# Kernel optimization log

Measured on AMD Instinct MI355X. Metric: run time of the kernel, lower is better.

## Reference

```python
import jax, jax.numpy as jnp
import numpy as np

NUM_INPUTS = 8
NUM_MFS = 3
NUM_RULES = NUM_MFS ** NUM_INPUTS  # 6561
BATCH = 8192


def setup_inputs() -> dict:
    key = jax.random.key(0)
    k1, k2, k3 = jax.random.split(key, 3)
    x = jax.random.normal(k1, (BATCH, NUM_INPUTS), dtype=jnp.float32)
    # one GaussianMF per input: centers ~ randn(num_mfs)
    centers = jax.random.normal(k2, (NUM_INPUTS, NUM_MFS), dtype=jnp.float32)
    # sigmas fixed buffer [0.3, 0.5, 0.7] shared across all inputs
    sigmas = jnp.array([0.3, 0.5, 0.7], dtype=jnp.float32)
    consequents = jax.random.normal(k3, (NUM_RULES, NUM_INPUTS + 1), dtype=jnp.float32)
    return {"x": x, "centers": centers, "sigmas": sigmas, "consequents": consequents}


def reference(x, centers, sigmas, consequents):
    B, nI = x.shape
    M = centers.shape[1]
    # Gaussian memberships: [B, nI, M]
    mu = jnp.exp(-0.5 * ((x[:, :, None] - centers[None, :, :]) / sigmas[None, None, :]) ** 2)
    # Rule strengths via successive outer products (lexicographic order matches
    # itertools.product(range(M), repeat=nI): first input varies slowest).
    s = mu[:, 0, :]  # [B, M]
    for j in range(1, nI):
        s = (s[:, :, None] * mu[:, j, None, :]).reshape(B, -1)  # [B, M^(j+1)]
    # s: [B, NUM_RULES]
    ones = jnp.ones((B, 1), dtype=x.dtype)
    xb = jnp.concatenate([x, ones], axis=1)  # [B, nI+1]
    rule_outputs = jnp.einsum('bi,ri->br', xb, consequents)  # [B, R]
    out = jnp.sum(s * rule_outputs, axis=1) / (jnp.sum(s, axis=1) + 1e-6)
    return out[:, None]
```

## Files before the change

### kernel.cpp

```cpp
#include <hip/hip_runtime.h>
#include <math.h>

#define BATCH   8192
#define NI      8
#define NM      3
#define NR      6561
#define NROWS   81
#define NL      81

__device__ __forceinline__ float sel3(const float* a, int i) {
    return (i == 0) ? a[0] : ((i == 1) ? a[1] : a[2]);
}

__global__ __launch_bounds__(256, 8) void sugeno_partial(
    const float* __restrict__ x,
    const float* __restrict__ centers,
    const float* __restrict__ sigmas,
    const float* __restrict__ cons,
    float* __restrict__ partial,
    int nchunk)
{
    const int b     = blockIdx.x * 256 + threadIdx.x;
    const int chunk = blockIdx.y;

    const float4* xv = reinterpret_cast<const float4*>(x + (size_t)b * NI);
    float4 xa = xv[0], xb4 = xv[1];
    float xr[NI];
    xr[0]=xa.x; xr[1]=xa.y; xr[2]=xa.z; xr[3]=xa.w;
    xr[4]=xb4.x; xr[5]=xb4.y; xr[6]=xb4.z; xr[7]=xb4.w;

    float inv[NM];
    #pragma unroll
    for (int m = 0; m < NM; ++m) {
        float s = sigmas[m];
        inv[m] = -0.5f / (s * s);
    }

    float mu[NI][NM];
    #pragma unroll
    for (int j = 0; j < NI; ++j) {
        #pragma unroll
        for (int m = 0; m < NM; ++m) {
            float d = xr[j] - centers[j * NM + m];
            mu[j][m] = __expf(d * d * inv[m]);
        }
    }

    const int rH0 = (chunk * NROWS) / nchunk;
    const int rH1 = ((chunk + 1) * NROWS) / nchunk;

    float V[9];
    #pragma unroll
    for (int i = 0; i < 9; ++i) V[i] = 0.0f;

    for (int rH = rH0; rH < rH1; ++rH) {
        int d0 = rH / 27, rem = rH - d0 * 27;
        int d1 = rem / 9;  rem -= d1 * 9;
        int d2 = rem / 3;
        int d3 = rem - d2 * 3;
        const float ph = sel3(mu[0], d0) * sel3(mu[1], d1)
                       * sel3(mu[2], d2) * sel3(mu[3], d3);
        const float* __restrict__ crow = cons + (size_t)rH * NL * 9;

        #pragma unroll
        for (int m4 = 0; m4 < 3; ++m4) {
            const float p4 = ph * mu[4][m4];
            #pragma unroll
            for (int m5 = 0; m5 < 3; ++m5) {
                const float p5 = p4 * mu[5][m5];
                #pragma unroll
                for (int m6 = 0; m6 < 3; ++m6) {
                    const float p6 = p5 * mu[6][m6];
                    #pragma unroll
                    for (int m7 = 0; m7 < 3; ++m7) {
                        const float s = p6 * mu[7][m7];
                        const float* cr = crow + (size_t)((((m4*3+m5)*3+m6)*3)+m7) * 9;
                        #pragma unroll
                        for (int i = 0; i < 9; ++i) V[i] += s * cr[i];
                    }
                }
            }
        }
    }

    const float numer = V[0]*xr[0] + V[1]*xr[1] + V[2]*xr[2] + V[3]*xr[3]
                      + V[4]*xr[4] + V[5]*xr[5] + V[6]*xr[6] + V[7]*xr[7]
                      + V[8];
    partial[(size_t)chunk * BATCH + b] = numer;
}

__global__ __launch_bounds__(256) void sugeno_reduce(
    const float* __restrict__ x,
    const float* __restrict__ centers,
    const float* __restrict__ sigmas,
    const float* __restrict__ partial,
    float* __restrict__ out,
    int nchunk)
{
    const int b = blockIdx.x * blockDim.x + threadIdx.x;
    if (b >= BATCH) return;

    const float4* xv = reinterpret_cast<const float4*>(x + (size_t)b * NI);
    float4 xa = xv[0], xb4 = xv[1];
    float xr[NI];
    xr[0]=xa.x; xr[1]=xa.y; xr[2]=xa.z; xr[3]=xa.w;
    xr[4]=xb4.x; xr[5]=xb4.y; xr[6]=xb4.z; xr[7]=xb4.w;

    float inv[NM];
    #pragma unroll
    for (int m = 0; m < NM; ++m) {
        float s = sigmas[m];
        inv[m] = -0.5f / (s * s);
    }

    float denom = 1.0f;
    #pragma unroll
    for (int j = 0; j < NI; ++j) {
        float srow = 0.0f;
        #pragma unroll
        for (int m = 0; m < NM; ++m) {
            float d = xr[j] - centers[j * NM + m];
            srow += __expf(d * d * inv[m]);
        }
        denom *= srow;
    }

    float numer = 0.0f;
    #pragma unroll 4
    for (int k = 0; k < nchunk; ++k)
        numer += partial[(size_t)k * BATCH + b];

    out[b] = numer / (denom + 1e-6f);
}

extern "C" void kernel_launch(void* const* d_in, const int* in_sizes, int n_in,
                              void* d_out, int out_size, void* d_ws, size_t ws_size,
                              hipStream_t stream)
{
    const float* x       = (const float*)d_in[0];
    const float* centers = (const float*)d_in[1];
    const float* sigmas  = (const float*)d_in[2];
    const float* cons    = (const float*)d_in[3];
    float* out           = (float*)d_out;
    float* partial       = (float*)d_ws;

    int nchunk = (int)(ws_size / ((size_t)BATCH * sizeof(float)));
    if (nchunk > NROWS) nchunk = NROWS;
    if (nchunk < 1)     nchunk = 1;

    dim3 grid1(BATCH / 256, nchunk, 1);
    sugeno_partial<<<grid1, dim3(256, 1, 1), 0, stream>>>(x, centers, sigmas, cons,
                                                          partial, nchunk);

    dim3 grid2(BATCH / 256, 1, 1);
    sugeno_reduce<<<grid2, dim3(256, 1, 1), 0, stream>>>(x, centers, sigmas,
                                                         partial, out, nchunk);
}
```

Before: 27.87 us.

## Fix one rule-row per block and split partial reduction across waves

The partial kernel now always launches 81 row-chunks (one high-order rule row per block), so each thread computes only the memberships it needs for that row instead of all 24 exponentials and the selection logic. Exponentials use exp2f with a pre-scaled constant. The reduce kernel spreads the 81-way sum over four waves per block and combines them through shared memory, giving more parallelism in the reduction. The change assumes the workspace can always hold 81 partial rows; the old code capped the chunk count by workspace size, and it writes more partial data than before.

```diff
diff --git a/kernel.cpp b/kernel.cpp
--- a/kernel.cpp
+++ b/kernel.cpp
@@ -4,24 +4,19 @@
 #define BATCH   8192
 #define NI      8
 #define NM      3
-#define NR      6561
 #define NROWS   81
 #define NL      81
+#define IL2C    (-0.72134752f)
 
-__device__ __forceinline__ float sel3(const float* a, int i) {
-    return (i == 0) ? a[0] : ((i == 1) ? a[1] : a[2]);
-}
-
-__global__ __launch_bounds__(256, 8) void sugeno_partial(
+__global__ __launch_bounds__(256) void sugeno_partial(
     const float* __restrict__ x,
     const float* __restrict__ centers,
     const float* __restrict__ sigmas,
     const float* __restrict__ cons,
-    float* __restrict__ partial,
-    int nchunk)
+    float* __restrict__ partial)
 {
-    const int b     = blockIdx.x * 256 + threadIdx.x;
-    const int chunk = blockIdx.y;
+    const int b  = blockIdx.x * 256 + threadIdx.x;
+    const int rH = blockIdx.y;
 
     const float4* xv = reinterpret_cast<const float4*>(x + (size_t)b * NI);
     float4 xa = xv[0], xb4 = xv[1];
@@ -29,55 +24,59 @@
     xr[0]=xa.x; xr[1]=xa.y; xr[2]=xa.z; xr[3]=xa.w;
     xr[4]=xb4.x; xr[5]=xb4.y; xr[6]=xb4.z; xr[7]=xb4.w;
 
-    float inv[NM];
+    float il2[NM];
     #pragma unroll
     for (int m = 0; m < NM; ++m) {
         float s = sigmas[m];
-        inv[m] = -0.5f / (s * s);
+        il2[m] = IL2C / (s * s);
     }
 
-    float mu[NI][NM];
+    const int d0 = rH / 27;
+    const int d1 = (rH / 9) % 3;
+    const int d2 = (rH / 3) % 3;
+    const int d3 = rH % 3;
+
+    float dd0 = xr[0] - centers[0 * NM + d0];
+    float dd1 = xr[1] - centers[1 * NM + d1];
+    float dd2 = xr[2] - centers[2 * NM + d2];
+    float dd3 = xr[3] - centers[3 * NM + d3];
+    float ph = exp2f(dd0 * dd0 * il2[d0]) * exp2f(dd1 * dd1 * il2[d1])
+             * exp2f(dd2 * dd2 * il2[d2]) * exp2f(dd3 * dd3 * il2[d3]);
+
+    float mu4[NM], mu5[NM], mu6[NM], mu7[NM];
     #pragma unroll
-    for (int j = 0; j < NI; ++j) {
-        #pragma unroll
-        for (int m = 0; m < NM; ++m) {
-            float d = xr[j] - centers[j * NM + m];
-            mu[j][m] = __expf(d * d * inv[m]);
-        }
+    for (int m = 0; m < NM; ++m) {
+        float e4 = xr[4] - centers[4 * NM + m];
+        float e5 = xr[5] - centers[5 * NM + m];
+        float e6 = xr[6] - centers[6 * NM + m];
+        float e7 = xr[7] - centers[7 * NM + m];
+        mu4[m] = exp2f(e4 * e4 * il2[m]);
+        mu5[m] = exp2f(e5 * e5 * il2[m]);
+        mu6[m] = exp2f(e6 * e6 * il2[m]);
+        mu7[m] = exp2f(e7 * e7 * il2[m]);
     }
 
-    const int rH0 = (chunk * NROWS) / nchunk;
-    const int rH1 = ((chunk + 1) * NROWS) / nchunk;
+    const float* __restrict__ crow = cons + (size_t)rH * NL * 9;
 
     float V[9];
     #pragma unroll
     for (int i = 0; i < 9; ++i) V[i] = 0.0f;
 
-    for (int rH = rH0; rH < rH1; ++rH) {
-        int d0 = rH / 27, rem = rH - d0 * 27;
-        int d1 = rem / 9;  rem -= d1 * 9;
-        int d2 = rem / 3;
-        int d3 = rem - d2 * 3;
-        const float ph = sel3(mu[0], d0) * sel3(mu[1], d1)
-                       * sel3(mu[2], d2) * sel3(mu[3], d3);
-        const float* __restrict__ crow = cons + (size_t)rH * NL * 9;
-
+    #pragma unroll
+    for (int m4 = 0; m4 < 3; ++m4) {
+        const float p4 = ph * mu4[m4];
         #pragma unroll
-        for (int m4 = 0; m4 < 3; ++m4) {
-            const float p4 = ph * mu[4][m4];
+        for (int m5 = 0; m5 < 3; ++m5) {
+            const float p5 = p4 * mu5[m5];
             #pragma unroll
-            for (int m5 = 0; m5 < 3; ++m5) {
-                const float p5 = p4 * mu[5][m5];
+            for (int m6 = 0; m6 < 3; ++m6) {
+                const float p6 = p5 * mu6[m6];
                 #pragma unroll
-                for (int m6 = 0; m6 < 3; ++m6) {
-                    const float p6 = p5 * mu[6][m6];
+                for (int m7 = 0; m7 < 3; ++m7) {
+                    const float s = p6 * mu7[m7];
+                    const float* cr = crow + (size_t)((((m4*3+m5)*3+m6)*3)+m7) * 9;
                     #pragma unroll
-                    for (int m7 = 0; m7 < 3; ++m7) {
-                        const float s = p6 * mu[7][m7];
-                        const float* cr = crow + (size_t)((((m4*3+m5)*3+m6)*3)+m7) * 9;
-                        #pragma unroll
-                        for (int i = 0; i < 9; ++i) V[i] += s * cr[i];
-                    }
+                    for (int i = 0; i < 9; ++i) V[i] += s * cr[i];
                 }
             }
         }
@@ -86,7 +85,7 @@
     const float numer = V[0]*xr[0] + V[1]*xr[1] + V[2]*xr[2] + V[3]*xr[3]
                       + V[4]*xr[4] + V[5]*xr[5] + V[6]*xr[6] + V[7]*xr[7]
                       + V[8];
-    partial[(size_t)chunk * BATCH + b] = numer;
+    partial[(size_t)rH * BATCH + b] = numer;
 }
 
 __global__ __launch_bounds__(256) void sugeno_reduce(
@@ -94,43 +93,49 @@
     const float* __restrict__ centers,
     const float* __restrict__ sigmas,
     const float* __restrict__ partial,
-    float* __restrict__ out,
-    int nchunk)
+    float* __restrict__ out)
 {
-    const int b = blockIdx.x * blockDim.x + threadIdx.x;
-    if (b >= BATCH) return;
+    __shared__ float red[4][64];
+    const int lane = threadIdx.x & 63;
+    const int w    = threadIdx.x >> 6;
+    const int b    = blockIdx.x * 64 + lane;
 
-    const float4* xv = reinterpret_cast<const float4*>(x + (size_t)b * NI);
-    float4 xa = xv[0], xb4 = xv[1];
-    float xr[NI];
-    xr[0]=xa.x; xr[1]=xa.y; xr[2]=xa.z; xr[3]=xa.w;
-    xr[4]=xb4.x; xr[5]=xb4.y; xr[6]=xb4.z; xr[7]=xb4.w;
+    float acc = 0.0f;
+    #pragma unroll 7
+    for (int k = w; k < NROWS; k += 4)
+        acc += partial[(size_t)k * BATCH + b];
+    red[w][lane] = acc;
+    __syncthreads();
 
-    float inv[NM];
-    #pragma unroll
-    for (int m = 0; m < NM; ++m) {
-        float s = sigmas[m];
-        inv[m] = -0.5f / (s * s);
-    }
+    if (w == 0) {
+        float numer = red[0][lane] + red[1][lane] + red[2][lane] + red[3][lane];
 
-    float denom = 1.0f;
-    #pragma unroll
-    for (int j = 0; j < NI; ++j) {
-        float srow = 0.0f;
+        const float4* xv = reinterpret_cast<const float4*>(x + (size_t)b * NI);
+        float4 xa = xv[0], xb4 = xv[1];
+        float xr[NI];
+        xr[0]=xa.x; xr[1]=xa.y; xr[2]=xa.z; xr[3]=xa.w;
+        xr[4]=xb4.x; xr[5]=xb4.y; xr[6]=xb4.z; xr[7]=xb4.w;
+
+        float il2[NM];
         #pragma unroll
         for (int m = 0; m < NM; ++m) {
-            float d = xr[j] - centers[j * NM + m];
-            srow += __expf(d * d * inv[m]);
+            float s = sigmas[m];
+            il2[m] = IL2C / (s * s);
         }
-        denom *= srow;
+
+        float denom = 1.0f;
+        #pragma unroll
+        for (int j = 0; j < NI; ++j) {
+            float srow = 0.0f;
+            #pragma unroll
+            for (int m = 0; m < NM; ++m) {
+                float d = xr[j] - centers[j * NM + m];
+                srow += exp2f(d * d * il2[m]);
+            }
+            denom *= srow;
+        }
+        out[b] = numer / (denom + 1e-6f);
     }
-
-    float numer = 0.0f;
-    #pragma unroll 4
-    for (int k = 0; k < nchunk; ++k)
-        numer += partial[(size_t)k * BATCH + b];
-
-    out[b] = numer / (denom + 1e-6f);
 }
 
 extern "C" void kernel_launch(void* const* d_in, const int* in_sizes, int n_in,
@@ -144,15 +149,8 @@
     float* out           = (float*)d_out;
     float* partial       = (float*)d_ws;
 
-    int nchunk = (int)(ws_size / ((size_t)BATCH * sizeof(float)));
-    if (nchunk > NROWS) nchunk = NROWS;
-    if (nchunk < 1)     nchunk = 1;
+    dim3 grid1(BATCH / 256, NROWS, 1);
+    sugeno_partial<<<grid1, dim3(256, 1, 1), 0, stream>>>(x, centers, sigmas, cons, partial);
 
-    dim3 grid1(BATCH / 256, nchunk, 1);
-    sugeno_partial<<<grid1, dim3(256, 1, 1), 0, stream>>>(x, centers, sigmas, cons,
-                                                          partial, nchunk);
-
-    dim3 grid2(BATCH / 256, 1, 1);
-    sugeno_reduce<<<grid2, dim3(256, 1, 1), 0, stream>>>(x, centers, sigmas,
-                                                         partial, out, nchunk);
+    sugeno_reduce<<<BATCH / 64, 256, 0, stream>>>(x, centers, sigmas, partial, out);
 }
```

New measurement: 32.81 us. 17.7% more time.
